# Performance work log

Hardware: AMD Instinct MI355X
Metric: run time of the kernel (lower is better)

Reference implementation:

```python
import jax, jax.numpy as jnp
import numpy as np

B, C, H, W = 8, 256, 128, 128
NW = 512  # n_weights (depthwise multiplier 2)
EPS = 1e-5
SPARSITY = 0.5


def setup_inputs() -> dict:
    key = jax.random.key(0)
    k_x, k_sign, k_mask, k_w1 = jax.random.split(key, 4)
    x = jax.random.normal(k_x, (B, C, H, W), dtype=jnp.float32)
    gamma = jnp.ones((C,), dtype=jnp.float32)
    beta = jnp.zeros((C,), dtype=jnp.float32)
    # frozen binary/sparse LBP depthwise weights in {-1, 0, +1}
    sign = jax.random.bernoulli(k_sign, 0.5, (NW, 1, 3, 3)).astype(jnp.float32) * 2.0 - 1.0
    inactive = jax.random.uniform(k_mask, (NW, 1, 3, 3)) > SPARSITY
    lbp_w = jnp.where(inactive, 0.0, sign)
    # 1x1 conv params (PyTorch default init scale)
    bound = 1.0 / np.sqrt(NW)
    w1 = jax.random.uniform(k_w1, (C, NW, 1, 1), minval=-bound, maxval=bound, dtype=jnp.float32)
    b1 = jnp.zeros((C,), dtype=jnp.float32)
    return {"x": x, "gamma": gamma, "beta": beta, "lbp_w": lbp_w, "w1": w1, "b1": b1}


def reference(x, gamma, beta, lbp_w, w1, b1):
    # BatchNorm2d in training mode: biased batch stats over (N, H, W)
    mean = jnp.mean(x, axis=(0, 2, 3), keepdims=True)
    var = jnp.var(x, axis=(0, 2, 3), keepdims=True)
    xn = (x - mean) * jax.lax.rsqrt(var + EPS)
    xn = xn * gamma[None, :, None, None] + beta[None, :, None, None]
    # depthwise 3x3 conv, padding=1, groups=C (depth multiplier NW//C)
    y = jax.lax.conv_general_dilated(
        xn, lbp_w, window_strides=(1, 1), padding=((1, 1), (1, 1)),
        dimension_numbers=("NCHW", "OIHW", "NCHW"), feature_group_count=C)
    y = jax.nn.relu(y)
    # 1x1 conv NW -> C plus bias, then residual add
    z = jax.lax.conv_general_dilated(
        y, w1, window_strides=(1, 1), padding=((0, 0), (0, 0)),
        dimension_numbers=("NCHW", "OIHW", "NCHW"))
    z = z + b1[None, :, None, None]
    return z + x
```

## Files before the change

kernel.cpp:

```cpp
#include <hip/hip_runtime.h>

#define B_ 8
#define C_ 256
#define H_ 128
#define W_ 128
#define NW_ 512
#define HW_ (H_*W_)
#define EPS_ 1e-5f

typedef __attribute__((ext_vector_type(8))) short bf16x8;
typedef __attribute__((ext_vector_type(4))) float f32x4;

__device__ __forceinline__ unsigned short f2bf(float f) {
  unsigned u = __float_as_uint(f);
  u += 0x7fffu + ((u >> 16) & 1u);
  return (unsigned short)(u >> 16);
}
__device__ __forceinline__ float bf2f(unsigned short h) {
  return __uint_as_float(((unsigned)h) << 16);
}
__device__ __forceinline__ float bflo(unsigned u) { return __uint_as_float(u << 16); }
__device__ __forceinline__ float bfhi(unsigned u) { return __uint_as_float(u & 0xffff0000u); }

__global__ __launch_bounds__(256)
void bn_partial(const float* __restrict__ x, float* __restrict__ psum,
                float* __restrict__ psq) {
  const int b = blockIdx.x, c = blockIdx.y, tid = threadIdx.x;
  const float4* p = (const float4*)(x + (size_t)(b*C_ + c) * HW_);
  float s = 0.f, s2 = 0.f;
  #pragma unroll
  for (int i = 0; i < 16; ++i) {
    float4 v = p[tid + i*256];
    s  += v.x + v.y + v.z + v.w;
    s2 += v.x*v.x + v.y*v.y + v.z*v.z + v.w*v.w;
  }
  #pragma unroll
  for (int off = 32; off > 0; off >>= 1) {
    s  += __shfl_down(s, off);
    s2 += __shfl_down(s2, off);
  }
  __shared__ float rs[4], rq[4];
  if ((tid & 63) == 0) { rs[tid >> 6] = s; rq[tid >> 6] = s2; }
  __syncthreads();
  if (tid == 0) {
    float S = rs[0]+rs[1]+rs[2]+rs[3], S2 = rq[0]+rq[1]+rq[2]+rq[3];
    psum[c*B_ + b] = S;
    psq [c*B_ + b] = S2;
  }
}

__global__ __launch_bounds__(256)
void bn_final(float* __restrict__ wsf, const float* __restrict__ gamma,
              const float* __restrict__ beta) {
  const int c = threadIdx.x;
  float S = 0.f, S2 = 0.f;
  #pragma unroll
  for (int b = 0; b < B_; ++b) { S += wsf[512 + c*B_ + b]; S2 += wsf[2560 + c*B_ + b]; }
  const float n = (float)(B_*HW_);
  float mean = S / n;
  float var  = S2 / n - mean*mean;
  float scl  = gamma[c] * rsqrtf(var + EPS_);
  wsf[c]       = scl;
  wsf[C_ + c]  = beta[c] - mean*scl;
}

__global__ __launch_bounds__(64)
void w1prep(const float* __restrict__ w1, ushort* __restrict__ w1f) {
  const int l15 = threadIdx.x & 15, quad = threadIdx.x >> 4;
  const int mtG = blockIdx.x >> 4, ks = blockIdx.x & 15;
  const float* src = w1 + (size_t)(mtG*16 + l15)*NW_ + ks*32 + quad*8;
  float4 f0 = *(const float4*)src, f1 = *(const float4*)(src + 4);
  union { unsigned u[4]; uint4 q; } cv;
  cv.u[0] = (unsigned)f2bf(f0.x) | ((unsigned)f2bf(f0.y) << 16);
  cv.u[1] = (unsigned)f2bf(f0.z) | ((unsigned)f2bf(f0.w) << 16);
  cv.u[2] = (unsigned)f2bf(f1.x) | ((unsigned)f2bf(f1.y) << 16);
  cv.u[3] = (unsigned)f2bf(f1.z) | ((unsigned)f2bf(f1.w) << 16);
  ((uint4*)w1f)[blockIdx.x*64 + threadIdx.x] = cv.q;
}

template<bool PREW1>
__global__ __launch_bounds__(256, 2)
void fused_mfma(const float* __restrict__ x, const float* __restrict__ lbpw,
                const float* __restrict__ w1raw, const ushort* __restrict__ w1f,
                const float* __restrict__ b1, const float* __restrict__ sc_sh,
                float* __restrict__ out) {
  const int tid  = threadIdx.x;
  const int b    = blockIdx.z;
  const int h0   = blockIdx.y * 4;
  const int w0   = blockIdx.x * 16;
  const int wave = tid >> 6;
  const int lane = tid & 63;
  const int l15  = lane & 15;
  const int quad = lane >> 4;

  __shared__ float  s_scale[C_];
  __shared__ float  s_shift[C_];
  __shared__ float  s_b1[C_];
  __shared__ __align__(16) float  s_xn[16][6][20];
  __shared__ __align__(16) ushort s_yT[64][40];
  __shared__ __align__(16) ushort s_wc[32][16];
  __shared__ __align__(16) ushort s_res[256][66];

  s_scale[tid] = sc_sh[tid];
  s_shift[tid] = sc_sh[C_ + tid];
  s_b1[tid]    = b1[tid];

  const int ccin = tid >> 4;
  const int ccol = tid & 15;

  f32x4 acc[4][4];
  #pragma unroll
  for (int mt = 0; mt < 4; ++mt)
    #pragma unroll
    for (int nt = 0; nt < 4; ++nt) {
      f32x4 z = {0.f, 0.f, 0.f, 0.f};
      acc[mt][nt] = z;
    }

  __syncthreads();

  #pragma unroll 1
  for (int kc = 0; kc < 16; ++kc) {
    const int c0 = kc * 16;
    const int o0 = kc * 32;

    for (int idx = tid; idx < 16*6*18; idx += 256) {
      const int cl  = idx / 108;
      const int rem = idx - cl * 108;
      const int r   = rem / 18;
      const int col = rem - r * 18;
      const int h = h0 + r - 1;
      const int w = w0 + col - 1;
      float v = 0.f;
      if (h >= 0 && h < H_ && w >= 0 && w < W_) {
        const float xv = x[((size_t)(b*C_ + c0 + cl)*H_ + h)*W_ + w];
        v = fmaf(xv, s_scale[c0 + cl], s_shift[c0 + cl]);
        if (r >= 1 && r <= 4 && col >= 1 && col <= 16)
          s_res[c0 + cl][(r-1)*16 + (col-1)] = f2bf(xv);
      }
      s_xn[cl][r][col] = v;
    }
    for (int idx = tid; idx < 32*9; idx += 256) {
      const int oo = idx / 9;
      const int j  = idx - oo * 9;
      s_wc[oo][j] = f2bf(lbpw[(size_t)(o0 + oo)*9 + j]);
    }
    __syncthreads();

    {
      float v[6][3];
      #pragma unroll
      for (int rr = 0; rr < 6; ++rr)
        #pragma unroll
        for (int dj = 0; dj < 3; ++dj)
          v[rr][dj] = s_xn[ccin][rr][ccol + dj];

      const uint4 qa = *(const uint4*)&s_wc[2*ccin][0];
      const uint4 qb = *(const uint4*)&s_wc[2*ccin + 1][0];
      const float wA[9] = { bflo(qa.x), bfhi(qa.x), bflo(qa.y), bfhi(qa.y),
                            bflo(qa.z), bfhi(qa.z), bflo(qa.w), bfhi(qa.w),
                            bf2f(s_wc[2*ccin][8]) };
      const float wB[9] = { bflo(qb.x), bfhi(qb.x), bflo(qb.y), bfhi(qb.y),
                            bflo(qb.z), bfhi(qb.z), bflo(qb.w), bfhi(qb.w),
                            bf2f(s_wc[2*ccin + 1][8]) };
      float a0[4] = {0.f,0.f,0.f,0.f}, a1[4] = {0.f,0.f,0.f,0.f};
      #pragma unroll
      for (int r = 0; r < 4; ++r)
        #pragma unroll
        for (int di = 0; di < 3; ++di)
          #pragma unroll
          for (int dj = 0; dj < 3; ++dj) {
            const float t = v[r + di][dj];
            a0[r] = fmaf(wA[di*3 + dj], t, a0[r]);
            a1[r] = fmaf(wB[di*3 + dj], t, a1[r]);
          }
      #pragma unroll
      for (int r = 0; r < 4; ++r) {
        const unsigned pk = (unsigned)f2bf(fmaxf(a0[r], 0.f)) |
                            ((unsigned)f2bf(fmaxf(a1[r], 0.f)) << 16);
        *(unsigned*)&s_yT[r*16 + ccol][2*ccin] = pk;
      }
    }
    __syncthreads();

    bf16x8 bfr[4];
    #pragma unroll
    for (int nt = 0; nt < 4; ++nt)
      bfr[nt] = *(const bf16x8*)&s_yT[nt*16 + l15][quad*8];

    #pragma unroll
    for (int mt = 0; mt < 4; ++mt) {
      bf16x8 afr;
      if constexpr (PREW1) {
        union { uint4 q; bf16x8 v; } cv;
        cv.q = *(const uint4*)(w1f + (size_t)(((wave*4 + mt)*16 + kc)*64 + lane)*8);
        afr = cv.v;
      } else {
        const float* wp = w1raw + (size_t)(wave*64 + mt*16 + l15)*NW_ + o0 + quad*8;
        const float4 f0 = *(const float4*)wp;
        const float4 f1 = *(const float4*)(wp + 4);
        union { unsigned u[4]; bf16x8 v; } cv;
        cv.u[0] = (unsigned)f2bf(f0.x) | ((unsigned)f2bf(f0.y) << 16);
        cv.u[1] = (unsigned)f2bf(f0.z) | ((unsigned)f2bf(f0.w) << 16);
        cv.u[2] = (unsigned)f2bf(f1.x) | ((unsigned)f2bf(f1.y) << 16);
        cv.u[3] = (unsigned)f2bf(f1.z) | ((unsigned)f2bf(f1.w) << 16);
        afr = cv.v;
      }
      #pragma unroll
      for (int nt = 0; nt < 4; ++nt)
        acc[mt][nt] = __builtin_amdgcn_mfma_f32_16x16x32_bf16(afr, bfr[nt], acc[mt][nt], 0, 0, 0);
    }
    __syncthreads();
  }

  #pragma unroll
  for (int mt = 0; mt < 4; ++mt) {
    #pragma unroll
    for (int nt = 0; nt < 4; ++nt) {
      const int h   = h0 + nt;
      const int wcl = w0 + l15;
      const int px  = nt*16 + l15;
      #pragma unroll
      for (int i = 0; i < 4; ++i) {
        const int ch = wave*64 + mt*16 + quad*4 + i;
        const float r = bf2f(s_res[ch][px]);
        out[((size_t)(b*C_ + ch)*H_ + h)*W_ + wcl] = acc[mt][nt][i] + s_b1[ch] + r;
      }
    }
  }
}

extern "C" void kernel_launch(void* const* d_in, const int* in_sizes, int n_in,
                              void* d_out, int out_size, void* d_ws, size_t ws_size,
                              hipStream_t stream) {
  const float* x     = (const float*)d_in[0];
  const float* gamma = (const float*)d_in[1];
  const float* beta  = (const float*)d_in[2];
  const float* lbpw  = (const float*)d_in[3];
  const float* w1    = (const float*)d_in[4];
  const float* b1    = (const float*)d_in[5];
  float* out = (float*)d_out;

  float* wsf = (float*)d_ws;
  ushort* w1f = (ushort*)((char*)d_ws + 18432);
  const bool pre = ws_size >= (size_t)(18432 + 262144);

  bn_partial<<<dim3(B_, C_), 256, 0, stream>>>(x, wsf + 512, wsf + 2560);
  bn_final<<<1, 256, 0, stream>>>(wsf, gamma, beta);

  dim3 grid(W_/16, H_/4, B_);
  if (pre) {
    w1prep<<<256, 64, 0, stream>>>(w1, w1f);
    fused_mfma<true><<<grid, 256, 0, stream>>>(x, lbpw, w1, w1f, b1, wsf, out);
  } else {
    fused_mfma<false><<<grid, 256, 0, stream>>>(x, lbpw, w1, w1f, b1, wsf, out);
  }
}
```

Baseline: 446.4 us.

## Restructure fused kernel with register prefetch, smaller LDS, and split BN reduction

The BN partial-statistics kernel now splits each (batch, channel) plane into four segments, giving 32 partials per channel and more blocks in flight. The fused kernel now processes 32 channels per iteration in 8 iterations, and prefetches the next chunk of x into registers while computing the current one. It stores normalized x as bf16, drops the large residual LDS buffer by re-reading x from global memory in the epilogue, and raises the occupancy hint to 3 blocks per SM. The aim is to hide global load latency, cut barriers and LDS footprint, and improve occupancy. The trade-off is extra register pressure and bf16 rounding of the normalized input.

Result: slower. 455.6 us (+2.0%).

```diff
diff --git a/kernel.cpp b/kernel.cpp
--- a/kernel.cpp
+++ b/kernel.cpp
@@ -19,17 +19,19 @@
 __device__ __forceinline__ float bf2f(unsigned short h) {
   return __uint_as_float(((unsigned)h) << 16);
 }
-__device__ __forceinline__ float bflo(unsigned u) { return __uint_as_float(u << 16); }
-__device__ __forceinline__ float bfhi(unsigned u) { return __uint_as_float(u & 0xffff0000u); }
+__device__ __forceinline__ float bflo(unsigned u){ return __uint_as_float(u << 16); }
+__device__ __forceinline__ float bfhi(unsigned u){ return __uint_as_float(u & 0xffff0000u); }
 
 __global__ __launch_bounds__(256)
 void bn_partial(const float* __restrict__ x, float* __restrict__ psum,
                 float* __restrict__ psq) {
-  const int b = blockIdx.x, c = blockIdx.y, tid = threadIdx.x;
-  const float4* p = (const float4*)(x + (size_t)(b*C_ + c) * HW_);
+  const int seg = blockIdx.x;
+  const int c   = blockIdx.y;
+  const int tid = threadIdx.x;
+  const float4* p = (const float4*)(x + (size_t)((seg >> 2)*C_ + c)*HW_ + (seg & 3)*4096);
   float s = 0.f, s2 = 0.f;
   #pragma unroll
-  for (int i = 0; i < 16; ++i) {
+  for (int i = 0; i < 4; ++i) {
     float4 v = p[tid + i*256];
     s  += v.x + v.y + v.z + v.w;
     s2 += v.x*v.x + v.y*v.y + v.z*v.z + v.w*v.w;
@@ -43,9 +45,8 @@
   if ((tid & 63) == 0) { rs[tid >> 6] = s; rq[tid >> 6] = s2; }
   __syncthreads();
   if (tid == 0) {
-    float S = rs[0]+rs[1]+rs[2]+rs[3], S2 = rq[0]+rq[1]+rq[2]+rq[3];
-    psum[c*B_ + b] = S;
-    psq [c*B_ + b] = S2;
+    psum[c*32 + seg] = rs[0]+rs[1]+rs[2]+rs[3];
+    psq [c*32 + seg] = rq[0]+rq[1]+rq[2]+rq[3];
   }
 }
 
@@ -55,13 +56,16 @@
   const int c = threadIdx.x;
   float S = 0.f, S2 = 0.f;
   #pragma unroll
-  for (int b = 0; b < B_; ++b) { S += wsf[512 + c*B_ + b]; S2 += wsf[2560 + c*B_ + b]; }
+  for (int j = 0; j < 32; ++j) {
+    S  += wsf[512 + c*32 + j];
+    S2 += wsf[512 + 8192 + c*32 + j];
+  }
   const float n = (float)(B_*HW_);
   float mean = S / n;
   float var  = S2 / n - mean*mean;
   float scl  = gamma[c] * rsqrtf(var + EPS_);
-  wsf[c]       = scl;
-  wsf[C_ + c]  = beta[c] - mean*scl;
+  wsf[c]      = scl;
+  wsf[C_ + c] = beta[c] - mean*scl;
 }
 
 __global__ __launch_bounds__(64)
@@ -79,7 +83,7 @@
 }
 
 template<bool PREW1>
-__global__ __launch_bounds__(256, 2)
+__global__ __launch_bounds__(256, 3)
 void fused_mfma(const float* __restrict__ x, const float* __restrict__ lbpw,
                 const float* __restrict__ w1raw, const ushort* __restrict__ w1f,
                 const float* __restrict__ b1, const float* __restrict__ sc_sh,
@@ -92,21 +96,12 @@
   const int lane = tid & 63;
   const int l15  = lane & 15;
   const int quad = lane >> 4;
-
-  __shared__ float  s_scale[C_];
-  __shared__ float  s_shift[C_];
-  __shared__ float  s_b1[C_];
-  __shared__ __align__(16) float  s_xn[16][6][20];
-  __shared__ __align__(16) ushort s_yT[64][40];
-  __shared__ __align__(16) ushort s_wc[32][16];
-  __shared__ __align__(16) ushort s_res[256][66];
-
-  s_scale[tid] = sc_sh[tid];
-  s_shift[tid] = sc_sh[C_ + tid];
-  s_b1[tid]    = b1[tid];
-
-  const int ccin = tid >> 4;
-  const int ccol = tid & 15;
+  const int cl   = tid >> 3;
+  const int sub  = tid & 7;
+
+  __shared__ __align__(16) ushort s_xn[32][6][24];
+  __shared__ __align__(16) ushort s_yT[64][72];
+  __shared__ __align__(16) float  s_wc[64][12];
 
   f32x4 acc[4][4];
   #pragma unroll
@@ -117,114 +112,142 @@
       acc[mt][nt] = z;
     }
 
-  __syncthreads();
+  float pv[6][3];
+  float psc, psh;
+  auto prefetch = [&](int k) {
+    const int ch = k*32 + cl;
+    psc = sc_sh[ch];
+    psh = sc_sh[C_ + ch];
+    const float* bp = x + (size_t)(b*C_ + ch) * HW_;
+    #pragma unroll
+    for (int r = 0; r < 6; ++r) {
+      const int h = h0 + r - 1;
+      #pragma unroll
+      for (int s = 0; s < 3; ++s) {
+        const int c = sub + s*8;
+        const int w = w0 + c - 1;
+        const bool ok = (h >= 0) && (h < H_) && (c < 18) && (w >= 0) && (w < W_);
+        pv[r][s] = ok ? bp[h*W_ + w] : 0.f;
+      }
+    }
+  };
+
+  prefetch(0);
 
   #pragma unroll 1
-  for (int kc = 0; kc < 16; ++kc) {
-    const int c0 = kc * 16;
-    const int o0 = kc * 32;
-
-    for (int idx = tid; idx < 16*6*18; idx += 256) {
-      const int cl  = idx / 108;
-      const int rem = idx - cl * 108;
-      const int r   = rem / 18;
-      const int col = rem - r * 18;
+  for (int k = 0; k < 8; ++k) {
+    if (k) __syncthreads();
+
+    #pragma unroll
+    for (int r = 0; r < 6; ++r) {
       const int h = h0 + r - 1;
-      const int w = w0 + col - 1;
-      float v = 0.f;
-      if (h >= 0 && h < H_ && w >= 0 && w < W_) {
-        const float xv = x[((size_t)(b*C_ + c0 + cl)*H_ + h)*W_ + w];
-        v = fmaf(xv, s_scale[c0 + cl], s_shift[c0 + cl]);
-        if (r >= 1 && r <= 4 && col >= 1 && col <= 16)
-          s_res[c0 + cl][(r-1)*16 + (col-1)] = f2bf(xv);
-      }
-      s_xn[cl][r][col] = v;
-    }
-    for (int idx = tid; idx < 32*9; idx += 256) {
-      const int oo = idx / 9;
-      const int j  = idx - oo * 9;
-      s_wc[oo][j] = f2bf(lbpw[(size_t)(o0 + oo)*9 + j]);
+      const bool hv = (h >= 0) && (h < H_);
+      #pragma unroll
+      for (int s = 0; s < 3; ++s) {
+        const int c = sub + s*8;
+        if (c < 18) {
+          const int w = w0 + c - 1;
+          const bool ok = hv && (w >= 0) && (w < W_);
+          s_xn[cl][r][c] = ok ? f2bf(fmaf(pv[r][s], psc, psh)) : (ushort)0;
+        }
+      }
+    }
+    {
+      const int oo = tid >> 2, j0 = 3*(tid & 3);
+      if (j0 < 9) {
+        const float* wp = lbpw + (size_t)(k*64 + oo)*9 + j0;
+        s_wc[oo][j0]   = wp[0];
+        s_wc[oo][j0+1] = wp[1];
+        s_wc[oo][j0+2] = wp[2];
+      }
     }
     __syncthreads();
 
+    if (k < 7) prefetch(k + 1);
+
     {
-      float v[6][3];
-      #pragma unroll
-      for (int rr = 0; rr < 6; ++rr)
-        #pragma unroll
-        for (int dj = 0; dj < 3; ++dj)
-          v[rr][dj] = s_xn[ccin][rr][ccol + dj];
-
-      const uint4 qa = *(const uint4*)&s_wc[2*ccin][0];
-      const uint4 qb = *(const uint4*)&s_wc[2*ccin + 1][0];
-      const float wA[9] = { bflo(qa.x), bfhi(qa.x), bflo(qa.y), bfhi(qa.y),
-                            bflo(qa.z), bfhi(qa.z), bflo(qa.w), bfhi(qa.w),
-                            bf2f(s_wc[2*ccin][8]) };
-      const float wB[9] = { bflo(qb.x), bfhi(qb.x), bflo(qb.y), bfhi(qb.y),
-                            bflo(qb.z), bfhi(qb.z), bflo(qb.w), bfhi(qb.w),
-                            bf2f(s_wc[2*ccin + 1][8]) };
-      float a0[4] = {0.f,0.f,0.f,0.f}, a1[4] = {0.f,0.f,0.f,0.f};
-      #pragma unroll
-      for (int r = 0; r < 4; ++r)
+      float v[6][4];
+      #pragma unroll
+      for (int r = 0; r < 6; ++r) {
+        const unsigned u0 = *(const unsigned*)&s_xn[cl][r][2*sub];
+        const unsigned u1 = *(const unsigned*)&s_xn[cl][r][2*sub + 2];
+        v[r][0] = bflo(u0); v[r][1] = bfhi(u0);
+        v[r][2] = bflo(u1); v[r][3] = bfhi(u1);
+      }
+      const float4 wa0 = *(const float4*)&s_wc[2*cl][0];
+      const float4 wa1 = *(const float4*)&s_wc[2*cl][4];
+      const float  wa8 = s_wc[2*cl][8];
+      const float4 wb0 = *(const float4*)&s_wc[2*cl + 1][0];
+      const float4 wb1 = *(const float4*)&s_wc[2*cl + 1][4];
+      const float  wb8 = s_wc[2*cl + 1][8];
+      const float wA[9] = {wa0.x, wa0.y, wa0.z, wa0.w, wa1.x, wa1.y, wa1.z, wa1.w, wa8};
+      const float wB[9] = {wb0.x, wb0.y, wb0.z, wb0.w, wb1.x, wb1.y, wb1.z, wb1.w, wb8};
+      #pragma unroll
+      for (int r = 0; r < 4; ++r) {
+        float y0[2] = {0.f, 0.f}, y1[2] = {0.f, 0.f};
         #pragma unroll
         for (int di = 0; di < 3; ++di)
           #pragma unroll
           for (int dj = 0; dj < 3; ++dj) {
-            const float t = v[r + di][dj];
-            a0[r] = fmaf(wA[di*3 + dj], t, a0[r]);
-            a1[r] = fmaf(wB[di*3 + dj], t, a1[r]);
+            const float wa = wA[di*3 + dj], wb = wB[di*3 + dj];
+            #pragma unroll
+            for (int cc = 0; cc < 2; ++cc) {
+              const float t = v[r + di][dj + cc];
+              y0[cc] = fmaf(wa, t, y0[cc]);
+              y1[cc] = fmaf(wb, t, y1[cc]);
+            }
           }
-      #pragma unroll
-      for (int r = 0; r < 4; ++r) {
-        const unsigned pk = (unsigned)f2bf(fmaxf(a0[r], 0.f)) |
-                            ((unsigned)f2bf(fmaxf(a1[r], 0.f)) << 16);
-        *(unsigned*)&s_yT[r*16 + ccol][2*ccin] = pk;
+        #pragma unroll
+        for (int cc = 0; cc < 2; ++cc) {
+          const unsigned pk = (unsigned)f2bf(fmaxf(y0[cc], 0.f)) |
+                              ((unsigned)f2bf(fmaxf(y1[cc], 0.f)) << 16);
+          *(unsigned*)&s_yT[r*16 + 2*sub + cc][2*cl] = pk;
+        }
       }
     }
     __syncthreads();
 
-    bf16x8 bfr[4];
-    #pragma unroll
-    for (int nt = 0; nt < 4; ++nt)
-      bfr[nt] = *(const bf16x8*)&s_yT[nt*16 + l15][quad*8];
-
-    #pragma unroll
-    for (int mt = 0; mt < 4; ++mt) {
-      bf16x8 afr;
-      if constexpr (PREW1) {
-        union { uint4 q; bf16x8 v; } cv;
-        cv.q = *(const uint4*)(w1f + (size_t)(((wave*4 + mt)*16 + kc)*64 + lane)*8);
-        afr = cv.v;
-      } else {
-        const float* wp = w1raw + (size_t)(wave*64 + mt*16 + l15)*NW_ + o0 + quad*8;
-        const float4 f0 = *(const float4*)wp;
-        const float4 f1 = *(const float4*)(wp + 4);
-        union { unsigned u[4]; bf16x8 v; } cv;
-        cv.u[0] = (unsigned)f2bf(f0.x) | ((unsigned)f2bf(f0.y) << 16);
-        cv.u[1] = (unsigned)f2bf(f0.z) | ((unsigned)f2bf(f0.w) << 16);
-        cv.u[2] = (unsigned)f2bf(f1.x) | ((unsigned)f2bf(f1.y) << 16);
-        cv.u[3] = (unsigned)f2bf(f1.z) | ((unsigned)f2bf(f1.w) << 16);
-        afr = cv.v;
-      }
+    #pragma unroll
+    for (int ks = 0; ks < 2; ++ks) {
+      bf16x8 bfr[4];
       #pragma unroll
       for (int nt = 0; nt < 4; ++nt)
-        acc[mt][nt] = __builtin_amdgcn_mfma_f32_16x16x32_bf16(afr, bfr[nt], acc[mt][nt], 0, 0, 0);
-    }
-    __syncthreads();
+        bfr[nt] = *(const bf16x8*)&s_yT[nt*16 + l15][ks*32 + quad*8];
+      #pragma unroll
+      for (int mt = 0; mt < 4; ++mt) {
+        bf16x8 afr;
+        if constexpr (PREW1) {
+          union { uint4 q; bf16x8 v; } cv;
+          cv.q = *(const uint4*)(w1f + (size_t)(((wave*4 + mt)*16 + (k*2 + ks))*64 + lane)*8);
+          afr = cv.v;
+        } else {
+          const float* wp = w1raw + (size_t)(wave*64 + mt*16 + l15)*NW_ + k*64 + ks*32 + quad*8;
+          const float4 f0 = *(const float4*)wp;
+          const float4 f1 = *(const float4*)(wp + 4);
+          union { unsigned u[4]; bf16x8 v; } cv;
+          cv.u[0] = (unsigned)f2bf(f0.x) | ((unsigned)f2bf(f0.y) << 16);
+          cv.u[1] = (unsigned)f2bf(f0.z) | ((unsigned)f2bf(f0.w) << 16);
+          cv.u[2] = (unsigned)f2bf(f1.x) | ((unsigned)f2bf(f1.y) << 16);
+          cv.u[3] = (unsigned)f2bf(f1.z) | ((unsigned)f2bf(f1.w) << 16);
+          afr = cv.v;
+        }
+        #pragma unroll
+        for (int nt = 0; nt < 4; ++nt)
+          acc[mt][nt] = __builtin_amdgcn_mfma_f32_16x16x32_bf16(afr, bfr[nt], acc[mt][nt], 0, 0, 0);
+      }
+    }
   }
 
   #pragma unroll
   for (int mt = 0; mt < 4; ++mt) {
     #pragma unroll
     for (int nt = 0; nt < 4; ++nt) {
-      const int h   = h0 + nt;
-      const int wcl = w0 + l15;
-      const int px  = nt*16 + l15;
+      const int h = h0 + nt;
       #pragma unroll
       for (int i = 0; i < 4; ++i) {
         const int ch = wave*64 + mt*16 + quad*4 + i;
-        const float r = bf2f(s_res[ch][px]);
-        out[((size_t)(b*C_ + ch)*H_ + h)*W_ + wcl] = acc[mt][nt][i] + s_b1[ch] + r;
+        const size_t idx = ((size_t)(b*C_ + ch)*H_ + h)*W_ + w0 + l15;
+        out[idx] = acc[mt][nt][i] + b1[ch] + x[idx];
       }
     }
   }
@@ -241,11 +264,11 @@
   const float* b1    = (const float*)d_in[5];
   float* out = (float*)d_out;
 
-  float* wsf = (float*)d_ws;
-  ushort* w1f = (ushort*)((char*)d_ws + 18432);
-  const bool pre = ws_size >= (size_t)(18432 + 262144);
-
-  bn_partial<<<dim3(B_, C_), 256, 0, stream>>>(x, wsf + 512, wsf + 2560);
+  float* wsf  = (float*)d_ws;
+  ushort* w1f = (ushort*)((char*)d_ws + 69632);
+  const bool pre = ws_size >= (size_t)(69632 + 262144);
+
+  bn_partial<<<dim3(32, C_), 256, 0, stream>>>(x, wsf + 512, wsf + 512 + 8192);
   bn_final<<<1, 256, 0, stream>>>(wsf, gamma, beta);
 
   dim3 grid(W_/16, H_/4, B_);
```
